# Performance work log

Measured on AMD Instinct MI355X. Metric: run time of the kernel, lower is better.

The kernel has to match this reference:

```python
import jax, jax.numpy as jnp
import numpy as np

B, S, D, H, FF = 1, 2048, 2048, 32, 8192
HD = D // H
SCALING = HD ** -0.5
WBITS, ABITS = 8, 8
NEG = jnp.finfo(jnp.float32).min


def ste_round(x):
    # straight-through estimator round
    return x + jax.lax.stop_gradient(jnp.round(x) - x)


def fake_quant(x, bits, axis):
    # min-max asymmetric fake quantization (OmniQuant-style dynamic quant)
    qmax = float(2 ** bits - 1)
    xmin = jnp.minimum(jnp.min(x, axis=axis, keepdims=True), 0.0)
    xmax = jnp.maximum(jnp.max(x, axis=axis, keepdims=True), 0.0)
    scale = jnp.maximum((xmax - xmin) / qmax, 1e-5)
    zp = jnp.round(-xmin / scale)
    q = jnp.clip(ste_round(x / scale) + zp, 0.0, qmax)
    return (q - zp) * scale


def qlinear(x, W, b):
    # QuantLinear: quantize activation per-token, weight per-output-channel
    xq = fake_quant(x, ABITS, -1)
    Wq = fake_quant(W, WBITS, 1)  # W: [out, in], per-row (output channel)
    return xq @ Wq.T + b


def layernorm(x, g, b):
    mu = jnp.mean(x, axis=-1, keepdims=True)
    var = jnp.var(x, axis=-1, keepdims=True)
    return (x - mu) * jax.lax.rsqrt(var + 1e-5) * g + b


def setup_inputs():
    key = jax.random.key(0)
    ks = jax.random.split(key, 16)
    w = lambda k, shape: (jax.random.normal(k, shape) * 0.02).astype(jnp.float32)
    hidden_states = jax.random.normal(ks[0], (B, S, D), dtype=jnp.float32)
    causal = jnp.tril(jnp.ones((S, S), dtype=bool))
    attention_mask = jnp.where(causal, 0.0, NEG)[None, None].astype(jnp.float32)
    attention_mask = jnp.broadcast_to(attention_mask, (B, 1, S, S))
    return {
        'hidden_states': hidden_states,
        'attention_mask': attention_mask,
        'Wq': w(ks[1], (D, D)), 'bq': jnp.zeros((D,), jnp.float32),
        'Wk': w(ks[2], (D, D)), 'bk': jnp.zeros((D,), jnp.float32),
        'Wv': w(ks[3], (D, D)), 'bv': jnp.zeros((D,), jnp.float32),
        'Wo': w(ks[4], (D, D)), 'bo': jnp.zeros((D,), jnp.float32),
        'ln1_g': jnp.ones((D,), jnp.float32), 'ln1_b': jnp.zeros((D,), jnp.float32),
        'W1': w(ks[5], (FF, D)), 'b1': jnp.zeros((FF,), jnp.float32),
        'W2': w(ks[6], (D, FF)), 'b2': jnp.zeros((D,), jnp.float32),
        'ln2_g': jnp.ones((D,), jnp.float32), 'ln2_b': jnp.zeros((D,), jnp.float32),
    }


def _split_heads(x):
    # [B,S,D] -> [B,H,S,HD]
    return x.reshape(B, S, H, HD).transpose(0, 2, 1, 3)


def _layer(hidden_states, attention_mask, Wq, bq, Wk, bk, Wv, bv, Wo, bo,
           ln1_g, ln1_b, W1, b1, W2, b2, ln2_g, ln2_b):
    # ---- self attention block (do_layer_norm_before=True) ----
    residual = hidden_states
    x = layernorm(hidden_states, ln1_g, ln1_b)

    q = qlinear(x, Wq, bq) * SCALING
    q = fake_quant(q, ABITS, -1)          # qkt_matmul.quant_x1
    k = qlinear(x, Wk, bk)
    k = fake_quant(k, ABITS, -1)          # qkt_matmul.quant_x2
    v = qlinear(x, Wv, bv)
    v = fake_quant(v, ABITS, -1)          # pv_matmul.quant_x2

    qh, kh, vh = _split_heads(q), _split_heads(k), _split_heads(v)
    scores = jnp.einsum('bhqd,bhkd->bhqk', qh, kh)  # [B,H,S,S]
    scores = scores + attention_mask
    scores = jnp.maximum(scores, NEG)
    probs = jax.nn.softmax(scores, axis=-1)
    probs = fake_quant(probs, ABITS, -1)  # pv_matmul.quant_x1
    ctx = jnp.einsum('bhqk,bhkd->bhqd', probs, vh)
    ctx = ctx.transpose(0, 2, 1, 3).reshape(B, S, D)
    attn_out = qlinear(ctx, Wo, bo)
    hidden_states = residual + attn_out

    # ---- FFN block ----
    residual = hidden_states
    x = layernorm(hidden_states, ln2_g, ln2_b)
    x = jax.nn.relu(qlinear(x, W1, b1))
    x = qlinear(x, W2, b2)
    return residual + x


def reference(hidden_states, attention_mask, Wq, bq, Wk, bk, Wv, bv, Wo, bo,
              ln1_g, ln1_b, W1, b1, W2, b2, ln2_g, ln2_b):
    return _layer(hidden_states, attention_mask, Wq, bq, Wk, bk, Wv, bv, Wo, bo,
                  ln1_g, ln1_b, W1, b1, W2, b2, ln2_g, ln2_b)
```

## Files before the change

### kernel.cpp

```cpp
#include <hip/hip_runtime.h>
#include <hip/hip_bf16.h>
#include <math.h>

#define S_LEN 2048
#define D_DIM 2048
#define H_NUM 32
#define HD_DIM 64
#define FF_DIM 8192
#define QMAX 255.0f

typedef __attribute__((ext_vector_type(4))) float f32x4;
typedef __attribute__((ext_vector_type(4))) int i32x4;
typedef __attribute__((ext_vector_type(8))) __bf16 bf16x8;
typedef unsigned short u16;
typedef signed char i8;

__device__ __forceinline__ u16 f32i_to_bf16(float v) {
  return (u16)(__float_as_uint(v) >> 16);
}
__device__ __forceinline__ u16 f32_to_bf16_rne(float v) {
  __bf16 b = (__bf16)v;
  return *(u16*)&b;
}
__device__ __forceinline__ float bf16_to_f32(u16 u) {
// ... 149 lines not shown
    S0row[row] = red[0] + red[1] + red[2] + red[3];
    S1row[row] = red[4] + red[5] + red[6] + red[7];
  }
}

__device__ __forceinline__ void wquant_body(const float* __restrict__ wr0,
                                            i8* __restrict__ wo,
                                            float* __restrict__ sc,
                                            float* __restrict__ zc,
                                            float* __restrict__ S0c,
                                            float* __restrict__ S1c,
                                            int row, int K) {
  __shared__ float red[8];
  const int tid = threadIdx.x;
  const float4* wr = (const float4*)wr0;
  const int K4 = K >> 2, H4 = K4 >> 1;
  float mn = 0.f, mx = 0.f;
  for (int i = tid; i < K4; i += 256) {
    float4 v = wr[i];
    mn = fminf(mn, fminf(fminf(v.x, v.y), fminf(v.z, v.w)));
    mx = fmaxf(mx, fmaxf(fmaxf(v.x, v.y), fmaxf(v.z, v.w)));
  }
  mn = wred_min(mn); mx = wred_max(mx);
  if ((tid & 63) == 0) { red[tid >> 6] = mn; red[4 + (tid >> 6)] = mx; }
  __syncthreads();
  mn = fminf(fminf(red[0], red[1]), fminf(red[2], red[3]));
  mx = fmaxf(fmaxf(red[4], red[5]), fmaxf(red[6], red[7]));
  float scale = fmaxf((mx - mn) / QMAX, 1e-5f);
  float zp = rintf(-mn / scale);
  if (tid == 0) { sc[row] = scale; zc[row] = 128.0f - zp; }
  float s0 = 0.f, s1 = 0.f;
  for (int i = tid; i < K4; i += 256) {
    float4 v = wr[i];
    float q0 = fminf(fmaxf(rintf(v.x / scale) + zp, 0.f), QMAX);
    float q1 = fminf(fmaxf(rintf(v.y / scale) + zp, 0.f), QMAX);
    float q2 = fminf(fmaxf(rintf(v.z / scale) + zp, 0.f), QMAX);
    float q3 = fminf(fmaxf(rintf(v.w / scale) + zp, 0.f), QMAX);
    *(int*)&wo[i * 4] = pack4_i8(q0, q1, q2, q3);
    float gs = q0 + q1 + q2 + q3 - 512.f;
    if (i < H4) s0 += gs; else s1 += gs;
  }
  __syncthreads();
  s0 = wred_sum(s0); s1 = wred_sum(s1);
  if ((tid & 63) == 0) { red[tid >> 6] = s0; red[4 + (tid >> 6)] = s1; }
  __syncthreads();
  if (tid == 0) {
    S0c[row] = red[0] + red[1] + red[2] + red[3];
    S1c[row] = red[4] + red[5] + red[6] + red[7];
  }
}

__global__ __launch_bounds__(256) void wquant_i8(const float* __restrict__ W,
                                                 i8* __restrict__ Wi,
                                                 float* __restrict__ sc,
                                                 float* __restrict__ zc,
                                                 float* __restrict__ S0c,
                                                 float* __restrict__ S1c, int K) {
  const int row = blockIdx.x;
  wquant_body(W + (size_t)row * K, Wi + (size_t)row * K, sc, zc, S0c, S1c, row, K);
}

__global__ __launch_bounds__(256) void wquant4_i8(
    const float* __restrict__ W0, i8* __restrict__ O0, float* s0, float* z0, float* a0, float* b0,
    const float* __restrict__ W1, i8* __restrict__ O1, float* s1, float* z1, float* a1, float* b1,
    const float* __restrict__ W2, i8* __restrict__ O2, float* s2, float* z2, float* a2, float* b2,
    const float* __restrict__ W3, i8* __restrict__ O3, float* s3, float* z3, float* a3, float* b3) {
  const int which = blockIdx.x >> 11;
  const int row = blockIdx.x & (D_DIM - 1);
  const float* W = (which == 0) ? W0 : (which == 1) ? W1 : (which == 2) ? W2 : W3;
  i8* O = (which == 0) ? O0 : (which == 1) ? O1 : (which == 2) ? O2 : O3;
  float* sc = (which == 0) ? s0 : (which == 1) ? s1 : (which == 2) ? s2 : s3;
  float* zc = (which == 0) ? z0 : (which == 1) ? z1 : (which == 2) ? z2 : z3;
  float* Sa = (which == 0) ? a0 : (which == 1) ? a1 : (which == 2) ? a2 : a3;
  float* Sb = (which == 0) ? b0 : (which == 1) ? b1 : (which == 2) ? b2 : b3;
  wquant_body(W + (size_t)row * D_DIM, O + (size_t)row * D_DIM, sc, zc, Sa, Sb, row, D_DIM);
}

__global__ __launch_bounds__(256) void requant3(
    const u16* __restrict__ qv, const float* __restrict__ tqmn, const float* __restrict__ tqmx,
    u16* __restrict__ qo, float* __restrict__ sqv,
    const u16* __restrict__ kv, const float* __restrict__ tkmn, const float* __restrict__ tkmx,
    u16* __restrict__ ko, float* __restrict__ skv,
    const u16* __restrict__ vv, const float* __restrict__ tvmn, const float* __restrict__ tvmx,
    u16* __restrict__ vo) {
  __shared__ float red[8];
  const int wh = blockIdx.x >> 11;
  const int row = blockIdx.x & (S_LEN - 1);
  const int tid = threadIdx.x;
  const u16* vals = (wh == 0) ? qv : (wh == 1) ? kv : vv;
  const float* tmn = (wh == 0) ? tqmn : (wh == 1) ? tkmn : tvmn;
  const float* tmx = (wh == 0) ? tqmx : (wh == 1) ? tkmx : tvmx;
  u16* out = (wh == 0) ? qo : (wh == 1) ? ko : vo;
  float* srow = (wh == 0) ? sqv : (wh == 1) ? skv : nullptr;
  const int value_mode = (wh == 2) ? 1 : 0;

  float mn = 0.f, mx = 0.f;
  if (tid < 32) {
    mn = tmn[(size_t)row * 32 + tid];
    mx = tmx[(size_t)row * 32 + tid];
  }
  mn = wred_min(mn); mx = wred_max(mx);
  if ((tid & 63) == 0) { red[tid >> 6] = mn; red[4 + (tid >> 6)] = mx; }
  __syncthreads();
  mn = fminf(fminf(red[0], red[1]), fminf(red[2], red[3]));
  mx = fmaxf(fmaxf(red[4], red[5]), fmaxf(red[6], red[7]));
  mn = fminf(mn, 0.f); mx = fmaxf(mx, 0.f);
  float scale = fmaxf((mx - mn) / QMAX, 1e-5f);
  float zp = rintf(-mn / scale);
  if (srow && tid == 0) srow[row] = scale;
  const ushort4* vr = (const ushort4*)(vals + (size_t)row * D_DIM);
  ushort4* orow = (ushort4*)(out + (size_t)row * D_DIM);
  for (int i = tid; i < D_DIM / 4; i += 256) {
    ushort4 u = vr[i];
    float q0 = fminf(fmaxf(rintf(bf16_to_f32(u.x) / scale) + zp, 0.f), QMAX) - zp;
    float q1 = fminf(fmaxf(rintf(bf16_to_f32(u.y) / scale) + zp, 0.f), QMAX) - zp;
    float q2 = fminf(fmaxf(rintf(bf16_to_f32(u.z) / scale) + zp, 0.f), QMAX) - zp;
    float q3 = fminf(fmaxf(rintf(bf16_to_f32(u.w) / scale) + zp, 0.f), QMAX) - zp;
    ushort4 o;
    if (value_mode) {
      o.x = f32_to_bf16_rne(q0 * scale); o.y = f32_to_bf16_rne(q1 * scale);
      o.z = f32_to_bf16_rne(q2 * scale); o.w = f32_to_bf16_rne(q3 * scale);
    } else {
      o.x = f32i_to_bf16(q0); o.y = f32i_to_bf16(q1);
      o.z = f32i_to_bf16(q2); o.w = f32i_to_bf16(q3);
    }
    orow[i] = o;
  }
}

__global__ __launch_bounds__(256) void requant_ff_i8(const u16* __restrict__ vals,
                                                     const float* __restrict__ tmx,
                                                     i8* __restrict__ out,
                                                     float* __restrict__ srow,
                                                     float* __restrict__ zrow,
                                                     float* __restrict__ S0row,
                                                     float* __restrict__ S1row) {
  __shared__ float red[8];
  const int row = blockIdx.x, tid = threadIdx.x;
  float mx = (tid < 128) ? tmx[(size_t)row * 128 + tid] : 0.f;
  mx = wred_max(mx);
  if ((tid & 63) == 0) red[tid >> 6] = mx;
  __syncthreads();
  mx = fmaxf(fmaxf(red[0], red[1]), fmaxf(red[2], red[3]));
  mx = fmaxf(mx, 0.f);
  float scale = fmaxf(mx / QMAX, 1e-5f);
  if (tid == 0) { srow[row] = scale; zrow[row] = 128.0f; }
  const ushort4* vr = (const ushort4*)(vals + (size_t)row * FF_DIM);
  const int N4 = FF_DIM >> 2;
  float s0 = 0.f, s1 = 0.f;
  for (int i = tid; i < N4; i += 256) {
    ushort4 u = vr[i];
    float q0 = fminf(fmaxf(rintf(bf16_to_f32(u.x) / scale), 0.f), QMAX);
    float q1 = fminf(fmaxf(rintf(bf16_to_f32(u.y) / scale), 0.f), QMAX);
    float q2 = fminf(fmaxf(rintf(bf16_to_f32(u.z) / scale), 0.f), QMAX);
    float q3 = fminf(fmaxf(rintf(bf16_to_f32(u.w) / scale), 0.f), QMAX);
    *(int*)&out[(size_t)row * FF_DIM + i * 4] = pack4_i8(q0, q1, q2, q3);
    float gs = q0 + q1 + q2 + q3 - 512.f;
    if (i < 1024) s0 += gs; else s1 += gs;
  }
  __syncthreads();
  s0 = wred_sum(s0); s1 = wred_sum(s1);
  if ((tid & 63) == 0) { red[tid >> 6] = s0; red[4 + (tid >> 6)] = s1; }
  __syncthreads();
  if (tid == 0) {
    S0row[row] = red[0] + red[1] + red[2] + red[3];
    S1row[row] = red[4] + red[5] + red[6] + red[7];
  }
}

__device__ __forceinline__ void gemm128_i8_db(
    const i8* __restrict__ A, const i8* __restrict__ B,
    int K, int bm, int bn, int k_begin, int k_end,
    i8* As, i8* Bs, i32x4 (&acc)[4][4]) {
  const int tid = threadIdx.x;
  const int wid = tid >> 6, lane = tid & 63;
  const int wr = wid >> 1, wc = wid & 1;
  const int lr = lane & 15, lk = lane >> 4;
  const int r0 = tid >> 2, c0 = (tid & 3) * 16;
  const int r1 = 64 + r0;
  const size_t ldsb0 = (size_t)(wid * 64) * 16;
  const size_t ldsb1 = (size_t)(256 + wid * 64) * 16;

  const i8* Ag0 = A + (size_t)(bm + r0) * K + c0;
  const i8* Ag1 = A + (size_t)(bm + r1) * K + c0;
  const i8* Bg0 = B + (size_t)(bn + r0) * K + c0;
  const i8* Bg1 = B + (size_t)(bn + r1) * K + c0;

  const int nt = (k_end - k_begin) >> 6;

#define STAGE_I8(t)                                   \
  {                                                   \
    const int _k = k_begin + (t) * 64;                \
    i8* _Ab = As + (size_t)((t) & 1) * 8192;          \
    i8* _Bb = Bs + (size_t)((t) & 1) * 8192;          \
    gload_lds16(Ag0 + _k, _Ab + ldsb0);               \
    gload_lds16(Ag1 + _k, _Ab + ldsb1);               \
    gload_lds16(Bg0 + _k, _Bb + ldsb0);               \
    gload_lds16(Bg1 + _k, _Bb + ldsb1);               \
  }

  STAGE_I8(0);
  __syncthreads();

  for (int t = 0; t < nt; ++t) {
    const i8* Ac = As + (size_t)(t & 1) * 8192;
    const i8* Bc = Bs + (size_t)(t & 1) * 8192;
    i32x4 af[4], bf[4];
#pragma unroll
    for (int mi = 0; mi < 4; ++mi)
      af[mi] = *(const i32x4*)&Ac[(size_t)(wr * 64 + mi * 16 + lr) * 64 + lk * 16];
#pragma unroll
    for (int ni = 0; ni < 4; ++ni)
      bf[ni] = *(const i32x4*)&Bc[(size_t)(wc * 64 + ni * 16 + lr) * 64 + lk * 16];
    if (t + 1 < nt) STAGE_I8(t + 1);
#pragma unroll
    for (int mi = 0; mi < 4; ++mi)
#pragma unroll
      for (int ni = 0; ni < 4; ++ni)
        acc[mi][ni] = __builtin_amdgcn_mfma_i32_16x16x64_i8(af[mi], bf[ni], acc[mi][ni], 0, 0, 0);
    __syncthreads();
  }
#undef STAGE_I8
}

__global__ __launch_bounds__(256) void gemm_qkv_i8(
    const i8* __restrict__ A, const float* __restrict__ sx, const float* __restrict__ zx,
    const float* __restrict__ Sx0, const float* __restrict__ Sx1,
    const i8* __restrict__ Bq, const float* __restrict__ sbq, const float* __restrict__ zbq,
    const float* __restrict__ Sq0, const float* __restrict__ Sq1,
    const float* __restrict__ biasq, u16* __restrict__ Cq,
    float* __restrict__ tqmn, float* __restrict__ tqmx,
    const i8* __restrict__ Bk, const float* __restrict__ sbk, const float* __restrict__ zbk,
    const float* __restrict__ Sk0, const float* __restrict__ Sk1,
    const float* __restrict__ biask, u16* __restrict__ Ck,
    float* __restrict__ tkmn, float* __restrict__ tkmx,
    const i8* __restrict__ Bv, const float* __restrict__ sbv, const float* __restrict__ zbv,
    const float* __restrict__ Sv0, const float* __restrict__ Sv1,
    const float* __restrict__ biasv, u16* __restrict__ Cv,
    float* __restrict__ tvmn, float* __restrict__ tvmx) {
  __shared__ __align__(16) i8 As[2 * 128 * 64], Bs[2 * 128 * 64];
  int bx, by; xcd_swz(bx, by);
  const int which = bx >> 4;
  const int bn = (bx & 15) * 128;
  const int bm = by * 128;
  const i8* B = (which == 0) ? Bq : (which == 1) ? Bk : Bv;
  const float* sb = (which == 0) ? sbq : (which == 1) ? sbk : sbv;
  const float* zb = (which == 0) ? zbq : (which == 1) ? zbk : zbv;
  const float* Sb0 = (which == 0) ? Sq0 : (which == 1) ? Sk0 : Sv0;
  const float* Sb1 = (which == 0) ? Sq1 : (which == 1) ? Sk1 : Sv1;
  const float* bias = (which == 0) ? biasq : (which == 1) ? biask : biasv;
  u16* C = (which == 0) ? Cq : (which == 1) ? Ck : Cv;
  float* tmn = (which == 0) ? tqmn : (which == 1) ? tkmn : tvmn;
  float* tmx = (which == 0) ? tqmx : (which == 1) ? tkmx : tvmx;
  const float alpha = (which == 0) ? 0.125f : 1.0f;

  i32x4 acc[4][4] = {};
  gemm128_i8_db(A, B, D_DIM, bm, bn, 0, D_DIM, As, Bs, acc);

  const int tid = threadIdx.x;
  const int wid = tid >> 6, lane = tid & 63;
  const int wr = wid >> 1, wc = wid & 1;
  const int lr = lane & 15, lk = lane >> 4;
  const int col0 = bn + wc * 64 + lr;
  const int rbase = bm + wr * 64 + lk * 4;
  const int tci = (bn >> 6) + wc;
  float sbc[4], zbc[4], Sbc[4], bc[4];
#pragma unroll
  for (int ni = 0; ni < 4; ++ni) {
    const int col = col0 + ni * 16;
    sbc[ni] = sb[col]; zbc[ni] = zb[col];
    Sbc[ni] = Sb0[col] + Sb1[col]; bc[ni] = bias[col];
  }
#pragma unroll
  for (int mi = 0; mi < 4; ++mi) {
#pragma unroll
    for (int r = 0; r < 4; ++r) {
      const int row = rbase + mi * 16 + r;
      const float sar = sx[row], zar = zx[row];
      const float Sar = Sx0[row] + Sx1[row];
      float v[4];
#pragma unroll
      for (int ni = 0; ni < 4; ++ni) {
        float ci = (float)acc[mi][ni][r] + zar * Sbc[ni] + zbc[ni] * Sar +
                   2048.0f * zar * zbc[ni];
        v[ni] = (sar * sbc[ni] * ci + bc[ni]) * alpha;
      }
#pragma unroll
      for (int ni = 0; ni < 4; ++ni)
        C[(size_t)row * D_DIM + col0 + ni * 16] = f32_to_bf16_rne(v[ni]);
      float mnv = fminf(fminf(v[0], v[1]), fminf(v[2], v[3]));
      float mxv = fmaxf(fmaxf(v[0], v[1]), fmaxf(v[2], v[3]));
      mnv = fminf(mnv, __shfl_xor(mnv, 1, 64)); mxv = fmaxf(mxv, __shfl_xor(mxv, 1, 64));
      mnv = fminf(mnv, __shfl_xor(mnv, 2, 64)); mxv = fmaxf(mxv, __shfl_xor(mxv, 2, 64));
      mnv = fminf(mnv, __shfl_xor(mnv, 4, 64)); mxv = fmaxf(mxv, __shfl_xor(mxv, 4, 64));
      mnv = fminf(mnv, __shfl_xor(mnv, 8, 64)); mxv = fmaxf(mxv, __shfl_xor(mxv, 8, 64));
      if (lr == 0) {
        tmn[(size_t)row * 32 + tci] = mnv;
        tmx[(size_t)row * 32 + tci] = mxv;
      }
    }
  }
}

__global__ __launch_bounds__(256) void gemm_w1_i8(
    const i8* __restrict__ A, const float* __restrict__ sx, const float* __restrict__ zx,
    const float* __restrict__ Sx0, const float* __restrict__ Sx1,
    const i8* __restrict__ B, const float* __restrict__ sb, const float* __restrict__ zb,
    const float* __restrict__ Sb0, const float* __restrict__ Sb1,
    const float* __restrict__ bias, u16* __restrict__ C, float* __restrict__ tmx) {
  __shared__ __align__(16) i8 As[2 * 128 * 64], Bs[2 * 128 * 64];
  int bx, by; xcd_swz(bx, by);
  const int bn = bx * 128, bm = by * 128;

  i32x4 acc[4][4] = {};
  gemm128_i8_db(A, B, D_DIM, bm, bn, 0, D_DIM, As, Bs, acc);

  const int tid = threadIdx.x;
  const int wid = tid >> 6, lane = tid & 63;
  const int wr = wid >> 1, wc = wid & 1;
  const int lr = lane & 15, lk = lane >> 4;
  const int col0 = bn + wc * 64 + lr;
  const int rbase = bm + wr * 64 + lk * 4;
  const int tci = (bn >> 6) + wc;
  float sbc[4], zbc[4], Sbc[4], bc[4];
#pragma unroll
  for (int ni = 0; ni < 4; ++ni) {
    const int col = col0 + ni * 16;
    sbc[ni] = sb[col]; zbc[ni] = zb[col];
    Sbc[ni] = Sb0[col] + Sb1[col]; bc[ni] = bias[col];
  }
#pragma unroll
  for (int mi = 0; mi < 4; ++mi) {
#pragma unroll
    for (int r = 0; r < 4; ++r) {
      const int row = rbase + mi * 16 + r;
      const float sar = sx[row], zar = zx[row];
      const float Sar = Sx0[row] + Sx1[row];
      float v[4];
#pragma unroll
      for (int ni = 0; ni < 4; ++ni) {
        float ci = (float)acc[mi][ni][r] + zar * Sbc[ni] + zbc[ni] * Sar +
                   2048.0f * zar * zbc[ni];
        v[ni] = fmaxf(sar * sbc[ni] * ci + bc[ni], 0.f);
      }
#pragma unroll
      for (int ni = 0; ni < 4; ++ni)
        C[(size_t)row * FF_DIM + col0 + ni * 16] = f32_to_bf16_rne(v[ni]);
      float mxv = fmaxf(fmaxf(v[0], v[1]), fmaxf(v[2], v[3]));
      mxv = fmaxf(mxv, __shfl_xor(mxv, 1, 64));
      mxv = fmaxf(mxv, __shfl_xor(mxv, 2, 64));
      mxv = fmaxf(mxv, __shfl_xor(mxv, 4, 64));
      mxv = fmaxf(mxv, __shfl_xor(mxv, 8, 64));
      if (lr == 0) tmx[(size_t)row * 128 + tci] = mxv;
    }
  }
}

__global__ __launch_bounds__(256) void gemm_splitk_i8(
    const i8* __restrict__ A, const float* __restrict__ sx, const float* __restrict__ zx,
    const float* __restrict__ Sx0, const float* __restrict__ Sx1,
    const i8* __restrict__ B, const float* __restrict__ sb, const float* __restrict__ zb,
    const float* __restrict__ Sb0, const float* __restrict__ Sb1,
    float* __restrict__ part, int N, int K) {
  __shared__ __align__(16) i8 As[2 * 128 * 64], Bs[2 * 128 * 64];
  int bx, by; xcd_swz(bx, by);
  const int bm = by * 128, bn = bx * 128;
  const int ks = blockIdx.z;
  const int kchunk = K >> 1;
  i32x4 acc[4][4] = {};
  gemm128_i8_db(A, B, K, bm, bn, ks * kchunk, (ks + 1) * kchunk, As, Bs, acc);

  const float* Sxz = ks ? Sx1 : Sx0;
  const float* Sbz = ks ? Sb1 : Sb0;
  const float kcf = (float)kchunk;
  float* dst = part + (size_t)ks * S_LEN * N;
  const int tid = threadIdx.x;
  const int wid = tid >> 6, lane = tid & 63;
  const int wr = wid >> 1, wc = wid & 1;
  const int lr = lane & 15, lk = lane >> 4;
  const int col0 = bn + wc * 64 + lr;
  const int rbase = bm + wr * 64 + lk * 4;
#pragma unroll
  for (int ni = 0; ni < 4; ++ni) {
    const int col = col0 + ni * 16;
    const float sbc = sb[col], zbc = zb[col], Sbc = Sbz[col];
#pragma unroll
    for (int mi = 0; mi < 4; ++mi)
#pragma unroll
      for (int r = 0; r < 4; ++r) {
        const int row = rbase + mi * 16 + r;
        const float zar = zx[row];
        float ci = (float)acc[mi][ni][r] + zar * Sbc + zbc * Sxz[row] + kcf * zar * zbc;
        dst[(size_t)row * N + col] = sx[row] * sbc * ci;
      }
  }
}

__global__ __launch_bounds__(256) void splitk_reduce(
    const float* __restrict__ part,
    const float* __restrict__ bias, const float* __restrict__ res,
    float* __restrict__ out, int N) {
  const size_t stride4 = (size_t)S_LEN * N / 4;
  const int n4 = N >> 2;
  for (size_t i = (size_t)blockIdx.x * 256 + threadIdx.x; i < stride4;
       i += (size_t)gridDim.x * 256) {
    float4 s = ((const float4*)part)[i];
    float4 p = ((const float4*)part)[i + stride4];
    s.x += p.x; s.y += p.y; s.z += p.z; s.w += p.w;
    float4 b4 = ((const float4*)bias)[i % n4];
    s.x += b4.x; s.y += b4.y; s.z += b4.z; s.w += b4.w;
    if (res) {
      float4 r = ((const float4*)res)[i];
      s.x += r.x; s.y += r.y; s.z += r.z; s.w += r.w;
    }
    ((float4*)out)[i] = s;
  }
}

__global__ __launch_bounds__(256) void splitk_reduce_ln(
    const float* __restrict__ part,
    const float* __restrict__ bias, const float* __restrict__ res,
    float* __restrict__ h2out,
    const float* __restrict__ g, const float* __restrict__ bvec,
    i8* __restrict__ out, float* __restrict__ srow, float* __restrict__ zrow,
    float* __restrict__ S0row, float* __restrict__ S1row) {
  __shared__ float red[8];
  const int row = blockIdx.x, tid = threadIdx.x;
  const float4* p0 = (const float4*)(part + (size_t)row * D_DIM);
  const float4* p1 = (const float4*)(part + (size_t)S_LEN * D_DIM + (size_t)row * D_DIM);
  const float4* rr = (const float4*)(res + (size_t)row * D_DIM);
  const float4* b4 = (const float4*)bias;
  const float4* g4 = (const float4*)g;
  const float4* e4 = (const float4*)bvec;

  float4 a0 = p0[tid], a1 = p0[tid + 256];
  float4 q0 = p1[tid], q1 = p1[tid + 256];
  float4 r0 = rr[tid], r1 = rr[tid + 256];
  float4 c0 = b4[tid], c1 = b4[tid + 256];
  float4 v0, v1;
  v0.x = a0.x + q0.x + c0.x + r0.x; v0.y = a0.y + q0.y + c0.y + r0.y;
  v0.z = a0.z + q0.z + c0.z + r0.z; v0.w = a0.w + q0.w + c0.w + r0.w;
  v1.x = a1.x + q1.x + c1.x + r1.x; v1.y = a1.y + q1.y + c1.y + r1.y;
  v1.z = a1.z + q1.z + c1.z + r1.z; v1.w = a1.w + q1.w + c1.w + r1.w;
  float* h2r = h2out + (size_t)row * D_DIM;
  *(float4*)&h2r[tid * 4] = v0;
  *(float4*)&h2r[1024 + tid * 4] = v1;

  float s = v0.x + v0.y + v0.z + v0.w + v1.x + v1.y + v1.z + v1.w;
  float ss = v0.x * v0.x + v0.y * v0.y + v0.z * v0.z + v0.w * v0.w +
             v1.x * v1.x + v1.y * v1.y + v1.z * v1.z + v1.w * v1.w;
  s = wred_sum(s); ss = wred_sum(ss);
  if ((tid & 63) == 0) { red[tid >> 6] = s; red[4 + (tid >> 6)] = ss; }
  __syncthreads();
  float mu = (red[0] + red[1] + red[2] + red[3]) / (float)D_DIM;
  float var = (red[4] + red[5] + red[6] + red[7]) / (float)D_DIM - mu * mu;
  float rstd = 1.0f / sqrtf(var + 1e-5f);
  __syncthreads();

  float mn = 0.f, mx = 0.f;
  float4 n0, n1;
  {
    float4 gg = g4[tid], bb = e4[tid];
    n0.x = (v0.x - mu) * rstd * gg.x + bb.x; n0.y = (v0.y - mu) * rstd * gg.y + bb.y;
    n0.z = (v0.z - mu) * rstd * gg.z + bb.z; n0.w = (v0.w - mu) * rstd * gg.w + bb.w;
    gg = g4[tid + 256]; bb = e4[tid + 256];
    n1.x = (v1.x - mu) * rstd * gg.x + bb.x; n1.y = (v1.y - mu) * rstd * gg.y + bb.y;
    n1.z = (v1.z - mu) * rstd * gg.z + bb.z; n1.w = (v1.w - mu) * rstd * gg.w + bb.w;
    mn = fminf(mn, fminf(fminf(n0.x, n0.y), fminf(n0.z, n0.w)));
    mn = fminf(mn, fminf(fminf(n1.x, n1.y), fminf(n1.z, n1.w)));
    mx = fmaxf(mx, fmaxf(fmaxf(n0.x, n0.y), fmaxf(n0.z, n0.w)));
    mx = fmaxf(mx, fmaxf(fmaxf(n1.x, n1.y), fmaxf(n1.z, n1.w)));
  }
  mn = wred_min(mn); mx = wred_max(mx);
  if ((tid & 63) == 0) { red[tid >> 6] = mn; red[4 + (tid >> 6)] = mx; }
  __syncthreads();
  mn = fminf(fminf(red[0], red[1]), fminf(red[2], red[3]));
  mx = fmaxf(fmaxf(red[4], red[5]), fmaxf(red[6], red[7]));
  float scale = fmaxf((mx - mn) / QMAX, 1e-5f);
  float zp = rintf(-mn / scale);
  if (tid == 0) { srow[row] = scale; zrow[row] = 128.0f - zp; }
  float q00 = fminf(fmaxf(rintf(n0.x / scale) + zp, 0.f), QMAX);
  float q01 = fminf(fmaxf(rintf(n0.y / scale) + zp, 0.f), QMAX);
  float q02 = fminf(fmaxf(rintf(n0.z / scale) + zp, 0.f), QMAX);
  float q03 = fminf(fmaxf(rintf(n0.w / scale) + zp, 0.f), QMAX);
  float q10 = fminf(fmaxf(rintf(n1.x / scale) + zp, 0.f), QMAX);
  float q11 = fminf(fmaxf(rintf(n1.y / scale) + zp, 0.f), QMAX);
  float q12 = fminf(fmaxf(rintf(n1.z / scale) + zp, 0.f), QMAX);
  float q13 = fminf(fmaxf(rintf(n1.w / scale) + zp, 0.f), QMAX);
  *(int*)&out[(size_t)row * D_DIM + tid * 4] = pack4_i8(q00, q01, q02, q03);
  *(int*)&out[(size_t)row * D_DIM + 1024 + tid * 4] = pack4_i8(q10, q11, q12, q13);
  float s0 = q00 + q01 + q02 + q03 - 512.f;
  float s1 = q10 + q11 + q12 + q13 - 512.f;
  __syncthreads();
  s0 = wred_sum(s0); s1 = wred_sum(s1);
  if ((tid & 63) == 0) { red[tid >> 6] = s0; red[4 + (tid >> 6)] = s1; }
  __syncthreads();
  if (tid == 0) {
    S0row[row] = red[0] + red[1] + red[2] + red[3];
    S1row[row] = red[4] + red[5] + red[6] + red[7];
  }
}

__global__ __launch_bounds__(256) void attn_ml(
    const u16* __restrict__ qi, const float* __restrict__ sq,
    const u16* __restrict__ ki, const float* __restrict__ sk,
    float* __restrict__ Mb, float* __restrict__ Lb) {
  __shared__ __align__(16) u16 Qs[64][72];
  __shared__ __align__(16) u16 Ks[64][72];
  const int bid = blockIdx.x;
  const int ti = (S_LEN / 64 - 1) - (bid >> 5);
  const int h = bid & (H_NUM - 1);
  const int i0 = ti * 64;
  const int tid = threadIdx.x;
  const int wid = tid >> 6, lane = tid & 63;
  const int lr = lane & 15, g = lane >> 4;
  const size_t hbase = (size_t)h * HD_DIM;

  const int r_a = tid >> 3, ch_a = tid & 7;
  const int r_b = 32 + r_a;

  for (int c = tid; c < 512; c += 256) {
    int r = c >> 3, ch = c & 7;
    *(float4*)&Qs[r][ch * 8] =
        *(const float4*)&qi[(size_t)(i0 + r) * D_DIM + hbase + ch * 8];
  }
  float sq4[4];
#pragma unroll
  for (int r = 0; r < 4; ++r) sq4[r] = sq[i0 + wid * 16 + g * 4 + r];
  __syncthreads();

  const int ntiles = i0 / 64 + 1;
  float m_r[4] = {-1e30f, -1e30f, -1e30f, -1e30f};
  float l_r[4] = {0.f, 0.f, 0.f, 0.f};

  float4 ka0 = *(const float4*)&ki[(size_t)r_a * D_DIM + hbase + ch_a * 8];
  float4 ka1 = *(const float4*)&ki[(size_t)r_b * D_DIM + hbase + ch_a * 8];
  for (int t = 0; t < ntiles; ++t) {
    __syncthreads();
    *(float4*)&Ks[r_a][ch_a * 8] = ka0;
    *(float4*)&Ks[r_b][ch_a * 8] = ka1;
    __syncthreads();
    if (t + 1 < ntiles) {
      const int jn = (t + 1) * 64;
      ka0 = *(const float4*)&ki[(size_t)(jn + r_a) * D_DIM + hbase + ch_a * 8];
      ka1 = *(const float4*)&ki[(size_t)(jn + r_b) * D_DIM + hbase + ch_a * 8];
    }

    bf16x8 aq0 = *(const bf16x8*)&Qs[wid * 16 + lr][g * 8];
    bf16x8 aq1 = *(const bf16x8*)&Qs[wid * 16 + lr][32 + g * 8];
    f32x4 accs[4] = {};
#pragma unroll
    for (int ni = 0; ni < 4; ++ni) {
      bf16x8 b0 = *(const bf16x8*)&Ks[ni * 16 + lr][g * 8];
      bf16x8 b1 = *(const bf16x8*)&Ks[ni * 16 + lr][32 + g * 8];
      accs[ni] = __builtin_amdgcn_mfma_f32_16x16x32_bf16(aq0, b0, accs[ni], 0, 0, 0);
      accs[ni] = __builtin_amdgcn_mfma_f32_16x16x32_bf16(aq1, b1, accs[ni], 0, 0, 0);
    }

    const int jt = t * 64;
    float sv[4][4];
#pragma unroll
    for (int ni = 0; ni < 4; ++ni) {
      const float skc = sk[jt + ni * 16 + lr];
#pragma unroll
      for (int r = 0; r < 4; ++r) sv[ni][r] = accs[ni][r] * sq4[r] * skc;
    }
    if (t == ntiles - 1) {
      const int jcol = jt + lr, irow = i0 + wid * 16 + g * 4;
#pragma unroll
      for (int ni = 0; ni < 4; ++ni)
#pragma unroll
        for (int r = 0; r < 4; ++r)
          if (jcol + ni * 16 > irow + r) sv[ni][r] = -1e30f;
    }
#pragma unroll
    for (int r = 0; r < 4; ++r) {
      float tmax = fmaxf(fmaxf(sv[0][r], sv[1][r]), fmaxf(sv[2][r], sv[3][r]));
      tmax = fmaxf(tmax, __shfl_xor(tmax, 1, 64));
      tmax = fmaxf(tmax, __shfl_xor(tmax, 2, 64));
      tmax = fmaxf(tmax, __shfl_xor(tmax, 4, 64));
      tmax = fmaxf(tmax, __shfl_xor(tmax, 8, 64));
      float mnew = fmaxf(m_r[r], tmax);
      float sum = __expf(sv[0][r] - mnew) + __expf(sv[1][r] - mnew) +
                  __expf(sv[2][r] - mnew) + __expf(sv[3][r] - mnew);
      sum += __shfl_xor(sum, 1, 64);
      sum += __shfl_xor(sum, 2, 64);
      sum += __shfl_xor(sum, 4, 64);
      sum += __shfl_xor(sum, 8, 64);
      l_r[r] = l_r[r] * __expf(m_r[r] - mnew) + sum;
      m_r[r] = mnew;
    }
  }

  if (lr == 0) {
#pragma unroll
    for (int r = 0; r < 4; ++r) {
      const int row = i0 + wid * 16 + g * 4 + r;
      Mb[(size_t)h * S_LEN + row] = m_r[r];
      Lb[(size_t)h * S_LEN + row] = l_r[r];
    }
  }
}

__global__ __launch_bounds__(256) void attn_pv(
    const u16* __restrict__ qi, const float* __restrict__ sq,
    const u16* __restrict__ ki, const float* __restrict__ sk,
    const u16* __restrict__ vf,
    const float* __restrict__ Mb, const float* __restrict__ Lb,
    float* __restrict__ ctx) {
  __shared__ __align__(16) u16 Qs[64][72];
  __shared__ __align__(16) u16 Ks[64][72];
  __shared__ __align__(16) u16 Ps[64][72];
  __shared__ __align__(16) u16 Vt[64][72];
  const int bid = blockIdx.x;
  const int ti = (S_LEN / 64 - 1) - (bid >> 5);
  const int h = bid & (H_NUM - 1);
  const int i0 = ti * 64;
  const int tid = threadIdx.x;
  const int wid = tid >> 6, lane = tid & 63;
  const int lr = lane & 15, g = lane >> 4;
  const size_t hbase = (size_t)h * HD_DIM;

  const int r_a = tid >> 3, ch_a = tid & 7;
  const int r_b = 32 + r_a;
  const int jr_v = tid & 63, ch_v = tid >> 6;

  for (int c = tid; c < 512; c += 256) {
    int r = c >> 3, ch = c & 7;
    *(float4*)&Qs[r][ch * 8] =
        *(const float4*)&qi[(size_t)(i0 + r) * D_DIM + hbase + ch * 8];
  }
  float sq4[4], m_r[4], qsc[4], idn[4];
#pragma unroll
  for (int r = 0; r < 4; ++r) {
    const int row = i0 + wid * 16 + g * 4 + r;
    sq4[r] = sq[row];
    m_r[r] = Mb[(size_t)h * S_LEN + row];
    float li = Lb[(size_t)h * S_LEN + row];
    float sc = fmaxf((1.0f / li) / QMAX, 1e-5f);
    qsc[r] = sc;
    idn[r] = 1.0f / (li * sc);
  }
  __syncthreads();

  const int ntiles = i0 / 64 + 1;
  f32x4 acco[4] = {};
  float4 kb0 = *(const float4*)&ki[(size_t)r_a * D_DIM + hbase + ch_a * 8];
  float4 kb1 = *(const float4*)&ki[(size_t)r_b * D_DIM + hbase + ch_a * 8];
  float4 vb0 = *(const float4*)&vf[(size_t)jr_v * D_DIM + hbase + ch_v * 8];
  float4 vb1 = *(const float4*)&vf[(size_t)jr_v * D_DIM + hbase + (4 + ch_v) * 8];
  for (int t = 0; t < ntiles; ++t) {
    __syncthreads();
    *(float4*)&Ks[r_a][ch_a * 8] = kb0;
    *(float4*)&Ks[r_b][ch_a * 8] = kb1;
    {
      const u16* v0 = (const u16*)&vb0;
      const u16* v1 = (const u16*)&vb1;
#pragma unroll
      for (int e = 0; e < 8; ++e) Vt[ch_v * 8 + e][jr_v] = v0[e];
#pragma unroll
      for (int e = 0; e < 8; ++e) Vt[(4 + ch_v) * 8 + e][jr_v] = v1[e];
    }
    __syncthreads();
    if (t + 1 < ntiles) {
      const int jn = (t + 1) * 64;
      kb0 = *(const float4*)&ki[(size_t)(jn + r_a) * D_DIM + hbase + ch_a * 8];
      kb1 = *(const float4*)&ki[(size_t)(jn + r_b) * D_DIM + hbase + ch_a * 8];
      vb0 = *(const float4*)&vf[(size_t)(jn + jr_v) * D_DIM + hbase + ch_v * 8];
      vb1 = *(const float4*)&vf[(size_t)(jn + jr_v) * D_DIM + hbase + (4 + ch_v) * 8];
    }

    bf16x8 aq0 = *(const bf16x8*)&Qs[wid * 16 + lr][g * 8];
    bf16x8 aq1 = *(const bf16x8*)&Qs[wid * 16 + lr][32 + g * 8];
    f32x4 accs[4] = {};
#pragma unroll
    for (int ni = 0; ni < 4; ++ni) {
      bf16x8 b0 = *(const bf16x8*)&Ks[ni * 16 + lr][g * 8];
      bf16x8 b1 = *(const bf16x8*)&Ks[ni * 16 + lr][32 + g * 8];
      accs[ni] = __builtin_amdgcn_mfma_f32_16x16x32_bf16(aq0, b0, accs[ni], 0, 0, 0);
      accs[ni] = __builtin_amdgcn_mfma_f32_16x16x32_bf16(aq1, b1, accs[ni], 0, 0, 0);
    }

    const int jt = t * 64;
    const bool diag = (t == ntiles - 1);
    const int jcol = jt + lr, irow = i0 + wid * 16 + g * 4;
#pragma unroll
    for (int ni = 0; ni < 4; ++ni) {
      const float skc = sk[jt + ni * 16 + lr];
#pragma unroll
      for (int r = 0; r < 4; ++r) {
        float s = accs[ni][r] * sq4[r] * skc;
        if (diag && (jcol + ni * 16 > irow + r)) s = -1e30f;
        float e = __expf(s - m_r[r]);
        float q8 = fminf(fmaxf(rintf(e * idn[r]), 0.f), QMAX);
        Ps[wid * 16 + g * 4 + r][ni * 16 + lr] = f32i_to_bf16(q8);
      }
    }

    bf16x8 ap0 = *(const bf16x8*)&Ps[wid * 16 + lr][g * 8];
    bf16x8 ap1 = *(const bf16x8*)&Ps[wid * 16 + lr][32 + g * 8];
#pragma unroll
    for (int ni = 0; ni < 4; ++ni) {
      bf16x8 b0 = *(const bf16x8*)&Vt[ni * 16 + lr][g * 8];
      bf16x8 b1 = *(const bf16x8*)&Vt[ni * 16 + lr][32 + g * 8];
      acco[ni] = __builtin_amdgcn_mfma_f32_16x16x32_bf16(ap0, b0, acco[ni], 0, 0, 0);
      acco[ni] = __builtin_amdgcn_mfma_f32_16x16x32_bf16(ap1, b1, acco[ni], 0, 0, 0);
    }
  }

#pragma unroll
  for (int ni = 0; ni < 4; ++ni)
#pragma unroll
    for (int r = 0; r < 4; ++r) {
      const int row = i0 + wid * 16 + g * 4 + r;
      ctx[(size_t)row * D_DIM + hbase + ni * 16 + lr] = acco[ni][r] * qsc[r];
    }
}

extern "C" void kernel_launch(void* const* d_in, const int* in_sizes, int n_in,
                              void* d_out, int out_size, void* d_ws, size_t ws_size,
                              hipStream_t stream) {
  (void)in_sizes; (void)n_in; (void)out_size;
  const float* hs  = (const float*)d_in[0];
  const float* Wq  = (const float*)d_in[2];
  const float* bq  = (const float*)d_in[3];
  const float* Wk  = (const float*)d_in[4];
  const float* bk  = (const float*)d_in[5];
  const float* Wv  = (const float*)d_in[6];
  const float* bv  = (const float*)d_in[7];
  const float* Wo  = (const float*)d_in[8];
  const float* bo  = (const float*)d_in[9];
  const float* g1  = (const float*)d_in[10];
  const float* be1 = (const float*)d_in[11];
  const float* W1  = (const float*)d_in[12];
  const float* bf1 = (const float*)d_in[13];
  const float* W2  = (const float*)d_in[14];
  const float* bf2 = (const float*)d_in[15];
  const float* g2  = (const float*)d_in[16];
  const float* be2 = (const float*)d_in[17];
  float* out = (float*)d_out;

  const size_t SD = (size_t)S_LEN * D_DIM;
  const size_t SF = (size_t)S_LEN * FF_DIM;
  const size_t HS = (size_t)H_NUM * S_LEN;

  char* p = (char*)d_ws;
  auto alloc = [&](size_t bytes) { char* r = p; p += (bytes + 255) & ~(size_t)255; return r; };

  float* h2   = (float*)alloc(SD * 4);
  float* sx   = (float*)alloc(S_LEN * 4);
  float* zx   = (float*)alloc(S_LEN * 4);
  float* Sx0  = (float*)alloc(S_LEN * 4);
  float* Sx1  = (float*)alloc(S_LEN * 4);
  float* sxf  = (float*)alloc(S_LEN * 4);
  float* zxf  = (float*)alloc(S_LEN * 4);
  float* Sf0  = (float*)alloc(S_LEN * 4);
  float* Sf1  = (float*)alloc(S_LEN * 4);
  float* sqv  = (float*)alloc(S_LEN * 4);
  float* skv  = (float*)alloc(S_LEN * 4);
  float* Mb   = (float*)alloc(HS * 4);
  float* Lbv  = (float*)alloc(HS * 4);
  float* swq = (float*)alloc(D_DIM * 4); float* zwq = (float*)alloc(D_DIM * 4);
  float* Sq0 = (float*)alloc(D_DIM * 4); float* Sq1 = (float*)alloc(D_DIM * 4);
  float* swk = (float*)alloc(D_DIM * 4); float* zwk = (float*)alloc(D_DIM * 4);
  float* Sk0 = (float*)alloc(D_DIM * 4); float* Sk1 = (float*)alloc(D_DIM * 4);
  float* swv = (float*)alloc(D_DIM * 4); float* zwv = (float*)alloc(D_DIM * 4);
  float* Sv0 = (float*)alloc(D_DIM * 4); float* Sv1 = (float*)alloc(D_DIM * 4);
  float* swo = (float*)alloc(D_DIM * 4); float* zwo = (float*)alloc(D_DIM * 4);
  float* So0 = (float*)alloc(D_DIM * 4); float* So1 = (float*)alloc(D_DIM * 4);
  float* sw1 = (float*)alloc(FF_DIM * 4); float* zw1 = (float*)alloc(FF_DIM * 4);
  float* S10 = (float*)alloc(FF_DIM * 4); float* S11 = (float*)alloc(FF_DIM * 4);
  float* sw2 = (float*)alloc(D_DIM * 4); float* zw2 = (float*)alloc(D_DIM * 4);
  float* S20 = (float*)alloc(D_DIM * 4); float* S21 = (float*)alloc(D_DIM * 4);
  float* tqmn = (float*)alloc(S_LEN * 32 * 4);
  float* tqmx = (float*)alloc(S_LEN * 32 * 4);
  float* tkmn = (float*)alloc(S_LEN * 32 * 4);
  float* tkmx = (float*)alloc(S_LEN * 32 * 4);
  float* tvmn = (float*)alloc(S_LEN * 32 * 4);
  float* tvmx = (float*)alloc(S_LEN * 32 * 4);
  float* tf1x = (float*)alloc(S_LEN * 128 * 4);
  i8* xi  = (i8*)alloc(SD);
  i8* wqi = (i8*)alloc(SD);
  i8* wki = (i8*)alloc(SD);
  i8* wvi = (i8*)alloc(SD);
  i8* woi = (i8*)alloc(SD);
  i8* w1i = (i8*)alloc(SF);
  i8* w2i = (i8*)alloc(SF);
  i8* f1i = (i8*)alloc(SF);
  char* arena = alloc(8 * SD * 2);
  u16* qv   = (u16*)arena;
  u16* kv   = qv + SD;
  u16* vv   = kv + SD;
  u16* qi8  = vv + SD;
  u16* ki8  = qi8 + SD;
  u16* vfb  = ki8 + SD;
  float* ctxb = (float*)(vfb + SD);
  float* pwo = (float*)arena;
  u16* f1v = (u16*)arena;
  float* pw2 = (float*)(arena + 4 * SD * 2);
  size_t need = (size_t)(p - (char*)d_ws);
  if (ws_size < need) return;

  dim3 blk(256);

  wquant4_i8<<<4 * D_DIM, blk, 0, stream>>>(
      Wq, wqi, swq, zwq, Sq0, Sq1,
      Wk, wki, swk, zwk, Sk0, Sk1,
      Wv, wvi, swv, zwv, Sv0, Sv1,
      Wo, woi, swo, zwo, So0, So1);
  wquant_i8<<<FF_DIM, blk, 0, stream>>>(W1, w1i, sw1, zw1, S10, S11, D_DIM);
  wquant_i8<<<D_DIM, blk, 0, stream>>>(W2, w2i, sw2, zw2, S20, S21, FF_DIM);

  ln_quant_i8<<<S_LEN, blk, 0, stream>>>(hs, g1, be1, xi, sx, zx, Sx0, Sx1);

  dim3 gqkv(3 * D_DIM / 128, S_LEN / 128);
  gemm_qkv_i8<<<gqkv, blk, 0, stream>>>(xi, sx, zx, Sx0, Sx1,
                                        wqi, swq, zwq, Sq0, Sq1, bq, qv, tqmn, tqmx,
                                        wki, swk, zwk, Sk0, Sk1, bk, kv, tkmn, tkmx,
                                        wvi, swv, zwv, Sv0, Sv1, bv, vv, tvmn, tvmx);

  requant3<<<3 * S_LEN, blk, 0, stream>>>(qv, tqmn, tqmx, qi8, sqv,
                                          kv, tkmn, tkmx, ki8, skv,
                                          vv, tvmn, tvmx, vfb);

  const int ga = (S_LEN / 64) * H_NUM;
  attn_ml<<<ga, blk, 0, stream>>>(qi8, sqv, ki8, skv, Mb, Lbv);
  attn_pv<<<ga, blk, 0, stream>>>(qi8, sqv, ki8, skv, vfb, Mb, Lbv, ctxb);

  act_quant_i8<<<S_LEN, blk, 0, stream>>>(ctxb, xi, sx, zx, Sx0, Sx1);

  dim3 gwo(D_DIM / 128, S_LEN / 128, 2);
  gemm_splitk_i8<<<gwo, blk, 0, stream>>>(xi, sx, zx, Sx0, Sx1,
                                          woi, swo, zwo, So0, So1, pwo, D_DIM, D_DIM);
  splitk_reduce_ln<<<S_LEN, blk, 0, stream>>>(pwo, bo, hs, h2, g2, be2,
                                              xi, sx, zx, Sx0, Sx1);

  dim3 gff(FF_DIM / 128, S_LEN / 128);
  gemm_w1_i8<<<gff, blk, 0, stream>>>(xi, sx, zx, Sx0, Sx1,
                                      w1i, sw1, zw1, S10, S11, bf1, f1v, tf1x);
  requant_ff_i8<<<S_LEN, blk, 0, stream>>>(f1v, tf1x, f1i, sxf, zxf, Sf0, Sf1);

  dim3 gw2(D_DIM / 128, S_LEN / 128, 2);
  gemm_splitk_i8<<<gw2, blk, 0, stream>>>(f1i, sxf, zxf, Sf0, Sf1,
                                          w2i, sw2, zw2, S20, S21, pw2, D_DIM, FF_DIM);
  splitk_reduce<<<2048, blk, 0, stream>>>(pw2, bf2, h2, out, D_DIM);
}
```

Measured before the change: 458.0 us.

## Use 4-way split-K with raw int partials and move dequant into reductions

The Wo and W2 split-K GEMMs now split K four ways instead of two, giving 1024 blocks instead of 512 to fill the CUs. The GEMM epilogue now writes raw int32 accumulators as float, and the zero-point correction and scaling move into the reduction kernels using the full-K sums. A separate set of row quant buffers (sy/zy) avoids overwriting sx while the reduce kernel still reads it. Launch bounds with a min-blocks hint of 4 are added. The trade-off is doubled partial-buffer traffic, since four fp32 partial planes are written and read.

```diff
diff --git a/kernel.cpp b/kernel.cpp
--- a/kernel.cpp
+++ b/kernel.cpp
@@ -475,7 +475,7 @@
   }
 }
 
-__global__ __launch_bounds__(256) void gemm_w1_i8(
+__global__ __launch_bounds__(256, 4) void gemm_w1_i8(
     const i8* __restrict__ A, const float* __restrict__ sx, const float* __restrict__ zx,
     const float* __restrict__ Sx0, const float* __restrict__ Sx1,
     const i8* __restrict__ B, const float* __restrict__ sb, const float* __restrict__ zb,
@@ -529,24 +529,18 @@
   }
 }
 
-__global__ __launch_bounds__(256) void gemm_splitk_i8(
-    const i8* __restrict__ A, const float* __restrict__ sx, const float* __restrict__ zx,
-    const float* __restrict__ Sx0, const float* __restrict__ Sx1,
-    const i8* __restrict__ B, const float* __restrict__ sb, const float* __restrict__ zb,
-    const float* __restrict__ Sb0, const float* __restrict__ Sb1,
-    float* __restrict__ part, int N, int K) {
+__global__ __launch_bounds__(256, 4) void gemm_splitk_i8(
+    const i8* __restrict__ A, const i8* __restrict__ B,
+    float* __restrict__ part, int K, int nsplit) {
   __shared__ __align__(16) i8 As[2 * 128 * 64], Bs[2 * 128 * 64];
   int bx, by; xcd_swz(bx, by);
   const int bm = by * 128, bn = bx * 128;
   const int ks = blockIdx.z;
-  const int kchunk = K >> 1;
+  const int kchunk = K / nsplit;
   i32x4 acc[4][4] = {};
   gemm128_i8_db(A, B, K, bm, bn, ks * kchunk, (ks + 1) * kchunk, As, Bs, acc);
 
-  const float* Sxz = ks ? Sx1 : Sx0;
-  const float* Sbz = ks ? Sb1 : Sb0;
-  const float kcf = (float)kchunk;
-  float* dst = part + (size_t)ks * S_LEN * N;
+  float* dst = part + (size_t)ks * S_LEN * D_DIM;
   const int tid = threadIdx.x;
   const int wid = tid >> 6, lane = tid & 63;
   const int wr = wid >> 1, wc = wid & 1;
@@ -556,42 +550,59 @@
 #pragma unroll
   for (int ni = 0; ni < 4; ++ni) {
     const int col = col0 + ni * 16;
-    const float sbc = sb[col], zbc = zb[col], Sbc = Sbz[col];
 #pragma unroll
     for (int mi = 0; mi < 4; ++mi)
 #pragma unroll
-      for (int r = 0; r < 4; ++r) {
-        const int row = rbase + mi * 16 + r;
-        const float zar = zx[row];
-        float ci = (float)acc[mi][ni][r] + zar * Sbc + zbc * Sxz[row] + kcf * zar * zbc;
-        dst[(size_t)row * N + col] = sx[row] * sbc * ci;
-      }
-  }
-}
-
-__global__ __launch_bounds__(256) void splitk_reduce(
+      for (int r = 0; r < 4; ++r)
+        dst[(size_t)(rbase + mi * 16 + r) * D_DIM + col] = (float)acc[mi][ni][r];
+  }
+}
+
+__global__ __launch_bounds__(256) void splitk_reduce4(
     const float* __restrict__ part,
-    const float* __restrict__ bias, const float* __restrict__ res,
-    float* __restrict__ out, int N) {
-  const size_t stride4 = (size_t)S_LEN * N / 4;
-  const int n4 = N >> 2;
-  for (size_t i = (size_t)blockIdx.x * 256 + threadIdx.x; i < stride4;
+    const float* __restrict__ sxa, const float* __restrict__ zxa,
+    const float* __restrict__ Sxa0, const float* __restrict__ Sxa1,
+    const float* __restrict__ sw, const float* __restrict__ zw,
+    const float* __restrict__ Sw0, const float* __restrict__ Sw1,
+    float Kf, const float* __restrict__ bias, const float* __restrict__ res,
+    float* __restrict__ out) {
+  const size_t st4 = (size_t)S_LEN * D_DIM / 4;
+  for (size_t i = (size_t)blockIdx.x * 256 + threadIdx.x; i < st4;
        i += (size_t)gridDim.x * 256) {
+    const int row = (int)(i >> 9);
+    const int c4 = (int)(i & 511);
     float4 s = ((const float4*)part)[i];
-    float4 p = ((const float4*)part)[i + stride4];
-    s.x += p.x; s.y += p.y; s.z += p.z; s.w += p.w;
-    float4 b4 = ((const float4*)bias)[i % n4];
-    s.x += b4.x; s.y += b4.y; s.z += b4.z; s.w += b4.w;
+    float4 p1 = ((const float4*)part)[i + st4];
+    float4 p2 = ((const float4*)part)[i + 2 * st4];
+    float4 p3 = ((const float4*)part)[i + 3 * st4];
+    s.x += p1.x + p2.x + p3.x; s.y += p1.y + p2.y + p3.y;
+    s.z += p1.z + p2.z + p3.z; s.w += p1.w + p2.w + p3.w;
+    const float sxr = sxa[row], zxr = zxa[row];
+    const float Sxr = Sxa0[row] + Sxa1[row];
+    float4 ws = ((const float4*)sw)[c4];
+    float4 wz = ((const float4*)zw)[c4];
+    float4 w0 = ((const float4*)Sw0)[c4];
+    float4 w1 = ((const float4*)Sw1)[c4];
+    float4 b4 = ((const float4*)bias)[c4];
+    float4 o;
+    o.x = sxr * ws.x * (s.x + zxr * (w0.x + w1.x) + wz.x * Sxr + Kf * zxr * wz.x) + b4.x;
+    o.y = sxr * ws.y * (s.y + zxr * (w0.y + w1.y) + wz.y * Sxr + Kf * zxr * wz.y) + b4.y;
+    o.z = sxr * ws.z * (s.z + zxr * (w0.z + w1.z) + wz.z * Sxr + Kf * zxr * wz.z) + b4.z;
+    o.w = sxr * ws.w * (s.w + zxr * (w0.w + w1.w) + wz.w * Sxr + Kf * zxr * wz.w) + b4.w;
     if (res) {
       float4 r = ((const float4*)res)[i];
-      s.x += r.x; s.y += r.y; s.z += r.z; s.w += r.w;
-    }
-    ((float4*)out)[i] = s;
+      o.x += r.x; o.y += r.y; o.z += r.z; o.w += r.w;
+    }
+    ((float4*)out)[i] = o;
   }
 }
 
 __global__ __launch_bounds__(256) void splitk_reduce_ln(
     const float* __restrict__ part,
+    const float* __restrict__ sxa, const float* __restrict__ zxa,
+    const float* __restrict__ Sxa0, const float* __restrict__ Sxa1,
+    const float* __restrict__ sw, const float* __restrict__ zw,
+    const float* __restrict__ Sw0, const float* __restrict__ Sw1,
     const float* __restrict__ bias, const float* __restrict__ res,
     float* __restrict__ h2out,
     const float* __restrict__ g, const float* __restrict__ bvec,
@@ -599,22 +610,36 @@
     float* __restrict__ S0row, float* __restrict__ S1row) {
   __shared__ float red[8];
   const int row = blockIdx.x, tid = threadIdx.x;
+  const size_t st = (size_t)S_LEN * D_DIM;
   const float4* p0 = (const float4*)(part + (size_t)row * D_DIM);
-  const float4* p1 = (const float4*)(part + (size_t)S_LEN * D_DIM + (size_t)row * D_DIM);
+  const float4* p1 = (const float4*)(part + st + (size_t)row * D_DIM);
+  const float4* p2 = (const float4*)(part + 2 * st + (size_t)row * D_DIM);
+  const float4* p3 = (const float4*)(part + 3 * st + (size_t)row * D_DIM);
   const float4* rr = (const float4*)(res + (size_t)row * D_DIM);
   const float4* b4 = (const float4*)bias;
   const float4* g4 = (const float4*)g;
   const float4* e4 = (const float4*)bvec;
 
-  float4 a0 = p0[tid], a1 = p0[tid + 256];
-  float4 q0 = p1[tid], q1 = p1[tid + 256];
-  float4 r0 = rr[tid], r1 = rr[tid + 256];
-  float4 c0 = b4[tid], c1 = b4[tid + 256];
+  const float sxr = sxa[row], zxr = zxa[row];
+  const float Sxr = Sxa0[row] + Sxa1[row];
+
   float4 v0, v1;
-  v0.x = a0.x + q0.x + c0.x + r0.x; v0.y = a0.y + q0.y + c0.y + r0.y;
-  v0.z = a0.z + q0.z + c0.z + r0.z; v0.w = a0.w + q0.w + c0.w + r0.w;
-  v1.x = a1.x + q1.x + c1.x + r1.x; v1.y = a1.y + q1.y + c1.y + r1.y;
-  v1.z = a1.z + q1.z + c1.z + r1.z; v1.w = a1.w + q1.w + c1.w + r1.w;
+#pragma unroll
+  for (int h = 0; h < 2; ++h) {
+    const int idx = tid + h * 256;
+    float4 a = p0[idx], q = p1[idx], u = p2[idx], w = p3[idx];
+    float4 ws = ((const float4*)sw)[idx];
+    float4 wz = ((const float4*)zw)[idx];
+    float4 s0 = ((const float4*)Sw0)[idx];
+    float4 s1 = ((const float4*)Sw1)[idx];
+    float4 bb = b4[idx], rv = rr[idx];
+    float4 o;
+    o.x = sxr * ws.x * (a.x + q.x + u.x + w.x + zxr * (s0.x + s1.x) + wz.x * Sxr + 2048.0f * zxr * wz.x) + bb.x + rv.x;
+    o.y = sxr * ws.y * (a.y + q.y + u.y + w.y + zxr * (s0.y + s1.y) + wz.y * Sxr + 2048.0f * zxr * wz.y) + bb.y + rv.y;
+    o.z = sxr * ws.z * (a.z + q.z + u.z + w.z + zxr * (s0.z + s1.z) + wz.z * Sxr + 2048.0f * zxr * wz.z) + bb.z + rv.z;
+    o.w = sxr * ws.w * (a.w + q.w + u.w + w.w + zxr * (s0.w + s1.w) + wz.w * Sxr + 2048.0f * zxr * wz.w) + bb.w + rv.w;
+    if (h == 0) v0 = o; else v1 = o;
+  }
   float* h2r = h2out + (size_t)row * D_DIM;
   *(float4*)&h2r[tid * 4] = v0;
   *(float4*)&h2r[1024 + tid * 4] = v1;
@@ -925,6 +950,10 @@
   float* zx   = (float*)alloc(S_LEN * 4);
   float* Sx0  = (float*)alloc(S_LEN * 4);
   float* Sx1  = (float*)alloc(S_LEN * 4);
+  float* sy   = (float*)alloc(S_LEN * 4);
+  float* zy   = (float*)alloc(S_LEN * 4);
+  float* Sy0  = (float*)alloc(S_LEN * 4);
+  float* Sy1  = (float*)alloc(S_LEN * 4);
   float* sxf  = (float*)alloc(S_LEN * 4);
   float* zxf  = (float*)alloc(S_LEN * 4);
   float* Sf0  = (float*)alloc(S_LEN * 4);
@@ -970,7 +999,7 @@
   float* ctxb = (float*)(vfb + SD);
   float* pwo = (float*)arena;
   u16* f1v = (u16*)arena;
-  float* pw2 = (float*)(arena + 4 * SD * 2);
+  float* pw2 = (float*)arena;
   size_t need = (size_t)(p - (char*)d_ws);
   if (ws_size < need) return;
 
@@ -1002,19 +1031,20 @@
 
   act_quant_i8<<<S_LEN, blk, 0, stream>>>(ctxb, xi, sx, zx, Sx0, Sx1);
 
-  dim3 gwo(D_DIM / 128, S_LEN / 128, 2);
-  gemm_splitk_i8<<<gwo, blk, 0, stream>>>(xi, sx, zx, Sx0, Sx1,
-                                          woi, swo, zwo, So0, So1, pwo, D_DIM, D_DIM);
-  splitk_reduce_ln<<<S_LEN, blk, 0, stream>>>(pwo, bo, hs, h2, g2, be2,
-                                              xi, sx, zx, Sx0, Sx1);
+  dim3 gwo(D_DIM / 128, S_LEN / 128, 4);
+  gemm_splitk_i8<<<gwo, blk, 0, stream>>>(xi, woi, pwo, D_DIM, 4);
+  splitk_reduce_ln<<<S_LEN, blk, 0, stream>>>(pwo, sx, zx, Sx0, Sx1,
+                                              swo, zwo, So0, So1, bo, hs, h2,
+                                              g2, be2, xi, sy, zy, Sy0, Sy1);
 
   dim3 gff(FF_DIM / 128, S_LEN / 128);
-  gemm_w1_i8<<<gff, blk, 0, stream>>>(xi, sx, zx, Sx0, Sx1,
+  gemm_w1_i8<<<gff, blk, 0, stream>>>(xi, sy, zy, Sy0, Sy1,
                                       w1i, sw1, zw1, S10, S11, bf1, f1v, tf1x);
   requant_ff_i8<<<S_LEN, blk, 0, stream>>>(f1v, tf1x, f1i, sxf, zxf, Sf0, Sf1);
 
-  dim3 gw2(D_DIM / 128, S_LEN / 128, 2);
-  gemm_splitk_i8<<<gw2, blk, 0, stream>>>(f1i, sxf, zxf, Sf0, Sf1,
-                                          w2i, sw2, zw2, S20, S21, pw2, D_DIM, FF_DIM);
-  splitk_reduce<<<2048, blk, 0, stream>>>(pw2, bf2, h2, out, D_DIM);
-}
+  dim3 gw2(D_DIM / 128, S_LEN / 128, 4);
+  gemm_splitk_i8<<<gw2, blk, 0, stream>>>(f1i, w2i, pw2, FF_DIM, 4);
+  splitk_reduce4<<<2048, blk, 0, stream>>>(pw2, sxf, zxf, Sf0, Sf1,
+                                           sw2, zw2, S20, S21, (float)FF_DIM,
+                                           bf2, h2, out);
+}
```

Result: faster. 421.1 us (-8.1%).
